# Performance work log

Measured on AMD Instinct MI355X. Metric: run time of the kernel, lower is better.

## Reference

```python
import jax, jax.numpy as jnp
import numpy as np

B, T, I = 16, 2048, 256   # batch, seq_len, input_size
H = 256                   # dcg hidden == trn hidden per layer
DF = 0.9                  # discount_factor


def _lstm_scan(x, Wih, bih, Whh, bhh, coeff):
    """LSTM scan over time with discount-coeff gating.
    x: [B,T,in], Wih: [4H,in], Whh: [4H,H], coeff: [B,T,1] (already zeroed at t=0).
    h_t = LSTMCell(x_t, h_{t-1}, c_{t-1}).h + coeff_t * h_{t-1}  (PyTorch gate order i,f,g,o).
    """
    xp = jnp.einsum('bti,gi->btg', x, Wih) + bih  # precompute input projections [B,T,4H]
    Hh = Whh.shape[1]
    h0 = jnp.zeros((x.shape[0], Hh), x.dtype)

    def step(carry, inp):
        h, c = carry
        xg, cf = inp
        g = xg + h @ Whh.T + bhh
        ii, ff, gg, oo = jnp.split(g, 4, axis=-1)
        cn = jax.nn.sigmoid(ff) * c + jax.nn.sigmoid(ii) * jnp.tanh(gg)
        hn = jax.nn.sigmoid(oo) * jnp.tanh(cn) + cf * h
        return (hn, cn), hn

    _, hs = jax.lax.scan(step, (h0, h0), (xp.swapaxes(0, 1), coeff.swapaxes(0, 1)))
    return hs.swapaxes(0, 1)  # [B,T,H]


def _forward(inputs, dWih_f, dWhh_f, dbih_f, dbhh_f, dWih_b, dWhh_b, dbih_b, dbhh_b,
             l0Wih_f, l0Whh_f, l0bih_f, l0bhh_f, l0Wih_b, l0Whh_b, l0bih_b, l0bhh_b,
             l1Wih_f, l1Whh_f, l1bih_f, l1bhh_f, l1Wih_b, l1Whh_b, l1bih_b, l1bhh_b,
             cw_f, cb_f, cw_b, cb_b):
    z = jnp.zeros(inputs.shape[:2] + (1,), inputs.dtype)
    # discount-coefficient generator: plain bidirectional LSTM (no gating)
    dof = _lstm_scan(inputs, dWih_f, dbih_f, dWhh_f, dbhh_f, z)
    dob = _lstm_scan(inputs[:, ::-1], dWih_b, dbih_b, dWhh_b, dbhh_b, z)[:, ::-1]
    fwc = DF * jax.nn.sigmoid(dof @ cw_f.T + cb_f)        # [B,T,1]
    bwc = DF * jax.nn.sigmoid(dob @ cw_b.T + cb_b)[:, ::-1]  # flipped, consumed in reversed time
    # coeff blending only applies for step index i > 0 in each direction's loop
    cf = fwc.at[:, 0].set(0.0)
    cb = bwc.at[:, 0].set(0.0)

    layers = [((l0Wih_f, l0bih_f, l0Whh_f, l0bhh_f), (l0Wih_b, l0bih_b, l0Whh_b, l0bhh_b)),
              ((l1Wih_f, l1bih_f, l1Whh_f, l1bhh_f), (l1Wih_b, l1bih_b, l1Whh_b, l1bhh_b))]
    x = inputs
    for pf, pb in layers:
        of = _lstm_scan(x, *pf, cf)
        ob = _lstm_scan(x[:, ::-1], *pb, cb)[:, ::-1]
        x = jnp.concatenate([of, ob], axis=-1)  # [B,T,2H]
    return x


def setup_inputs():
    key = jax.random.key(0)
    ki = iter(jax.random.split(key, 64))
    d = {"inputs": jax.random.normal(next(ki), (B, T, I), dtype=jnp.float32)}
    for pre, ind in [("d", I), ("l0", I), ("l1", 2 * H)]:
        for dr in ("f", "b"):
            d[f"{pre}Wih_{dr}"] = 0.05 * jax.random.normal(next(ki), (4 * H, ind), dtype=jnp.float32)
            d[f"{pre}Whh_{dr}"] = 0.05 * jax.random.normal(next(ki), (4 * H, H), dtype=jnp.float32)
            d[f"{pre}bih_{dr}"] = jnp.zeros((4 * H,), jnp.float32)
            d[f"{pre}bhh_{dr}"] = jnp.zeros((4 * H,), jnp.float32)
    for dr in ("f", "b"):
        d[f"cw_{dr}"] = 0.05 * jax.random.normal(next(ki), (1, H), dtype=jnp.float32)
        d[f"cb_{dr}"] = jnp.zeros((1,), jnp.float32)
    return d


def reference(inputs, dWih_f, dWhh_f, dbih_f, dbhh_f, dWih_b, dWhh_b, dbih_b, dbhh_b,
              l0Wih_f, l0Whh_f, l0bih_f, l0bhh_f, l0Wih_b, l0Whh_b, l0bih_b, l0bhh_b,
              l1Wih_f, l1Whh_f, l1bih_f, l1bhh_f, l1Wih_b, l1Whh_b, l1bih_b, l1bhh_b,
              cw_f, cb_f, cw_b, cb_b):
    return _forward(inputs, dWih_f, dWhh_f, dbih_f, dbhh_f, dWih_b, dWhh_b, dbih_b, dbhh_b,
                    l0Wih_f, l0Whh_f, l0bih_f, l0bhh_f, l0Wih_b, l0Whh_b, l0bih_b, l0bhh_b,
                    l1Wih_f, l1Whh_f, l1bih_f, l1bhh_f, l1Wih_b, l1Whh_b, l1bih_b, l1bhh_b,
                    cw_f, cb_f, cw_b, cb_b)
```

## Files before the change

kernel.cpp:

```cpp
#include <hip/hip_runtime.h>

typedef unsigned short ushort;
typedef unsigned int uint32;
typedef unsigned long long ull;
typedef __attribute__((ext_vector_type(8))) short bf16x8;
typedef __attribute__((ext_vector_type(4))) float f32x4;

#define BATCH 16
#define TT 2048
#define HID 256

__device__ __forceinline__ ushort f2bf(float f) {
  union { float f; uint32 u; } v; v.f = f;
  uint32 r = v.u + 0x7FFFu + ((v.u >> 16) & 1u);
  return (ushort)(r >> 16);
}
__device__ __forceinline__ float bf2f(ushort u) {
  union { uint32 u; float f; } v; v.u = ((uint32)u) << 16; return v.f;
}
__device__ __forceinline__ float sigm(float x) { return 1.0f / (1.0f + __expf(-x)); }
__device__ __forceinline__ float tanh_fast(float x) { return 1.0f - 2.0f / (__expf(2.0f * x) + 1.0f); }

__global__ void prep_kernel(
    const float* __restrict__ x,
    const float* __restrict__ l1Wih_f, const float* __restrict__ l1Wih_b,
    const float* __restrict__ dbih_f, const float* __restrict__ dbhh_f,
    const float* __restrict__ dbih_b, const float* __restrict__ dbhh_b,
    const float* __restrict__ l0bih_f, const float* __restrict__ l0bhh_f,
    const float* __restrict__ l0bih_b, const float* __restrict__ l0bhh_b,
    const float* __restrict__ l1bih_f, const float* __restrict__ l1bhh_f,
    const float* __restrict__ l1bih_b, const float* __restrict__ l1bhh_b,
    ushort* __restrict__ xbf, ushort* __restrict__ wC,
    float* __restrict__ biasA, float* __restrict__ biasB, float* __restrict__ biasC)
{
  int g = blockIdx.x * blockDim.x + threadIdx.x;
  int str = gridDim.x * blockDim.x;
  for (int i = g; i < (BATCH * TT * 256) / 4; i += str) {
    float4 v = ((const float4*)x)[i];
    ushort4 o; o.x = f2bf(v.x); o.y = f2bf(v.y); o.z = f2bf(v.z); o.w = f2bf(v.w);
    ((ushort4*)xbf)[i] = o;
  }
  for (int i = g; i < 2048 * 512; i += str)
    wC[i] = f2bf(i < 1024 * 512 ? l1Wih_f[i] : l1Wih_b[i - 1024 * 512]);
  for (int i = g; i < 2048; i += str) {
    biasA[i] = i < 1024 ? dbih_f[i] + dbhh_f[i] : dbih_b[i - 1024] + dbhh_b[i - 1024];
    biasB[i] = i < 1024 ? l0bih_f[i] + l0bhh_f[i] : l0bih_b[i - 1024] + l0bhh_b[i - 1024];
    biasC[i] = i < 1024 ? l1bih_f[i] + l1bhh_f[i] : l1bih_b[i - 1024] + l1bhh_b[i - 1024];
  }
}

__global__ __launch_bounds__(256) void gemm_xp(
    const ushort* __restrict__ A, const ushort* __restrict__ B, int K,
    const float* __restrict__ bias, ushort* __restrict__ xp)
{
  __shared__ __align__(16) ushort lA[128 * 64];
  __shared__ __align__(16) ushort lB[128 * 64];
  const int tid = threadIdx.x;
  const int lane = tid & 63, wv = tid >> 6;
  const int lo = lane & 15, hi = lane >> 4;
  const int wr = wv >> 1, wc = wv & 1;
  const int bm = blockIdx.y * 128, bn = blockIdx.x * 128;

  f32x4 acc[4][4] = {};

  const int nk = K >> 6;
  for (int kt = 0; kt < nk; ++kt) {
    uint4 ra[4], rb[4];
#pragma unroll
    for (int i = 0; i < 4; ++i) {
      int slot = i * 256 + tid;
      int r = slot >> 3, c8 = slot & 7;
      ra[i] = *(const uint4*)(A + (size_t)(bm + r) * K + kt * 64 + c8 * 8);
      rb[i] = *(const uint4*)(B + (size_t)(bn + r) * K + kt * 64 + c8 * 8);
    }
    __syncthreads();
#pragma unroll
    for (int i = 0; i < 4; ++i) {
      int slot = i * 256 + tid;
      int r = slot >> 3, c8 = slot & 7;
      int boff = r * 128 + ((c8 ^ (r & 7)) << 4);
      *(uint4*)((char*)lA + boff) = ra[i];
      *(uint4*)((char*)lB + boff) = rb[i];
    }
    __syncthreads();
#pragma unroll
    for (int kk = 0; kk < 2; ++kk) {
      bf16x8 fa[4], fb[4];
#pragma unroll
      for (int mt = 0; mt < 4; ++mt) {
        int r = wr * 64 + mt * 16 + lo;
        int c8 = kk * 4 + hi;
        fa[mt] = *(const bf16x8*)((const char*)lA + r * 128 + ((c8 ^ (r & 7)) << 4));
      }
#pragma unroll
      for (int nt = 0; nt < 4; ++nt) {
        int r = wc * 64 + nt * 16 + lo;
        int c8 = kk * 4 + hi;
        fb[nt] = *(const bf16x8*)((const char*)lB + r * 128 + ((c8 ^ (r & 7)) << 4));
      }
#pragma unroll
      for (int mt = 0; mt < 4; ++mt)
#pragma unroll
        for (int nt = 0; nt < 4; ++nt)
          acc[mt][nt] = __builtin_amdgcn_mfma_f32_16x16x32_bf16(fa[mt], fb[nt], acc[mt][nt], 0, 0, 0);
    }
  }
#pragma unroll
  for (int nt = 0; nt < 4; ++nt) {
    int n = bn + wc * 64 + nt * 16 + lo;
    float bv = bias[n];
    int dirn = n >> 10;
    int c = n & 1023;
    int gate = c >> 8;
    int u = c & 255;
    size_t base = (size_t)dirn * ((size_t)BATCH * TT * 1024) + (size_t)(u >> 1) * 8 + gate * 2;
#pragma unroll
    for (int mt = 0; mt < 4; ++mt) {
#pragma unroll
      for (int r = 0; r < 4; ++r) {
        float val = acc[mt][nt][r] + bv;
        uint32 h16 = f2bf(val);
        uint32 p16 = (uint32)__shfl_xor((int)h16, 1);
        if (!(lo & 1)) {
          int m = bm + wr * 64 + mt * 16 + hi * 4 + r;
          *(uint32*)(xp + base + (size_t)m * 1024) = h16 | (p16 << 16);
        }
      }
    }
  }
}

template <int MODE>
__device__ __forceinline__ void scan_fly(
    const ushort* __restrict__ xbf,
    const float* __restrict__ WihF, const float* __restrict__ WihB,
    const float* __restrict__ WhhF, const float* __restrict__ WhhB,
    const float* __restrict__ biasAll,
    const float* ldsCW, float cbias,
    ull* __restrict__ coefT,
    ull* __restrict__ hst_base,
    ushort* __restrict__ outBf,
    const int dir, const int w, const int tid)
{
  const int lane = tid & 63, wv = tid >> 6;
  const int lo = lane & 15, hi = lane >> 4;

  const float* Wih = dir ? WihB : WihF;
  const float* Whh = dir ? WhhB : WhhF;
  ull* hst = hst_base + dir * (2 * 2048);
  ull* coefD = coefT + (size_t)dir * TT * 16;

  const int unit = w * 64 + wv * 16 + lo;
  const int b0 = hi * 4;

  bf16x8 wih[4][8], whh[4][8];
#pragma unroll
  for (int gt = 0; gt < 4; ++gt) {
    const float* r1 = Wih + (size_t)(gt * HID + unit) * HID;
    const float* r2 = Whh + (size_t)(gt * HID + unit) * HID;
#pragma unroll
    for (int kt = 0; kt < 8; ++kt) {
      bf16x8 f1, f2;
#pragma unroll
      for (int j = 0; j < 8; ++j) {
        f1[j] = (short)f2bf(r1[kt * 32 + hi * 8 + j]);
        f2[j] = (short)f2bf(r2[kt * 32 + hi * 8 + j]);
      }
      wih[gt][kt] = f1; whh[gt][kt] = f2;
    }
  }
  float biasv[4];
#pragma unroll
  for (int gt = 0; gt < 4; ++gt) biasv[gt] = biasAll[dir * 1024 + gt * 256 + unit];

  float hprev[4] = {0, 0, 0, 0}, cprev[4] = {0, 0, 0, 0};
  float co[4] = {0, 0, 0, 0};

  uint4 xn[8];
  {
    const int t0 = dir ? (TT - 1) : 0;
    const ushort* p = xbf + ((size_t)lo * TT + t0) * 256 + hi * 8;
#pragma unroll
    for (int kt = 0; kt < 8; ++kt) xn[kt] = *(const uint4*)(p + kt * 32);
  }

  bf16x8 af[8];

  for (int s = 0; s < TT; ++s) {
    bf16x8 xa[8];
#pragma unroll
    for (int kt = 0; kt < 8; ++kt) {
      union { uint4 u; bf16x8 v; } t; t.u = xn[kt]; xa[kt] = t.v;
    }
    f32x4 acc[4];
#pragma unroll
    for (int gt = 0; gt < 4; ++gt) {
      acc[gt] = (f32x4){biasv[gt], biasv[gt], biasv[gt], biasv[gt]};
      acc[gt] = __builtin_amdgcn_mfma_f32_16x16x32_bf16(xa[0], wih[gt][0], acc[gt], 0, 0, 0);
      acc[gt] = __builtin_amdgcn_mfma_f32_16x16x32_bf16(xa[1], wih[gt][1], acc[gt], 0, 0, 0);
      acc[gt] = __builtin_amdgcn_mfma_f32_16x16x32_bf16(xa[2], wih[gt][2], acc[gt], 0, 0, 0);
      acc[gt] = __builtin_amdgcn_mfma_f32_16x16x32_bf16(xa[3], wih[gt][3], acc[gt], 0, 0, 0);
      acc[gt] = __builtin_amdgcn_mfma_f32_16x16x32_bf16(xa[4], wih[gt][4], acc[gt], 0, 0, 0);
      acc[gt] = __builtin_amdgcn_mfma_f32_16x16x32_bf16(xa[5], wih[gt][5], acc[gt], 0, 0, 0);
      acc[gt] = __builtin_amdgcn_mfma_f32_16x16x32_bf16(xa[6], wih[gt][6], acc[gt], 0, 0, 0);
      acc[gt] = __builtin_amdgcn_mfma_f32_16x16x32_bf16(xa[7], wih[gt][7], acc[gt], 0, 0, 0);
    }

    if (s + 1 < TT) {
      const int tn = dir ? (TT - 2 - s) : (s + 1);
      const ushort* p = xbf + ((size_t)lo * TT + tn) * 256 + hi * 8;
#pragma unroll
      for (int kt = 0; kt < 8; ++kt) xn[kt] = *(const uint4*)(p + kt * 32);
    }

    if (s > 0) {
      const ull* bp = hst + (s & 1) * 2048 + hi * 64 + lo;
      const ull* cp = coefD + (size_t)s * 16 + b0;
      const uint32 su = (uint32)s;
      while (true) {
        uint32 bad = 0;
#pragma unroll
        for (int kt = 0; kt < 8; ++kt) {
          ull w0 = __hip_atomic_load(bp + kt * 256 +  0, __ATOMIC_RELAXED, __HIP_MEMORY_SCOPE_AGENT);
          ull w1 = __hip_atomic_load(bp + kt * 256 + 16, __ATOMIC_RELAXED, __HIP_MEMORY_SCOPE_AGENT);
          ull w2 = __hip_atomic_load(bp + kt * 256 + 32, __ATOMIC_RELAXED, __HIP_MEMORY_SCOPE_AGENT);
          ull w3 = __hip_atomic_load(bp + kt * 256 + 48, __ATOMIC_RELAXED, __HIP_MEMORY_SCOPE_AGENT);
          union { bf16x8 v; uint32 d[4]; } t;
          t.d[0] = (uint32)w0; t.d[1] = (uint32)w1; t.d[2] = (uint32)w2; t.d[3] = (uint32)w3;
          af[kt] = t.v;
          bad |= ((uint32)(w0 >> 32)) ^ su; bad |= ((uint32)(w1 >> 32)) ^ su;
          bad |= ((uint32)(w2 >> 32)) ^ su; bad |= ((uint32)(w3 >> 32)) ^ su;
        }
        if (MODE == 1) {
          ull c0 = __hip_atomic_load(cp + 0, __ATOMIC_RELAXED, __HIP_MEMORY_SCOPE_AGENT);
          ull c1 = __hip_atomic_load(cp + 1, __ATOMIC_RELAXED, __HIP_MEMORY_SCOPE_AGENT);
          ull c2 = __hip_atomic_load(cp + 2, __ATOMIC_RELAXED, __HIP_MEMORY_SCOPE_AGENT);
          ull c3 = __hip_atomic_load(cp + 3, __ATOMIC_RELAXED, __HIP_MEMORY_SCOPE_AGENT);
          bad |= ((uint32)(c0 >> 32)) ^ (su + 1); bad |= ((uint32)(c1 >> 32)) ^ (su + 1);
          bad |= ((uint32)(c2 >> 32)) ^ (su + 1); bad |= ((uint32)(c3 >> 32)) ^ (su + 1);
          co[0] = __uint_as_float((uint32)c0); co[1] = __uint_as_float((uint32)c1);
          co[2] = __uint_as_float((uint32)c2); co[3] = __uint_as_float((uint32)c3);
        }
        if (__all(bad == 0)) break;
      }
#pragma unroll
      for (int gt = 0; gt < 4; ++gt) {
        acc[gt] = __builtin_amdgcn_mfma_f32_16x16x32_bf16(af[0], whh[gt][0], acc[gt], 0, 0, 0);
        acc[gt] = __builtin_amdgcn_mfma_f32_16x16x32_bf16(af[1], whh[gt][1], acc[gt], 0, 0, 0);
        acc[gt] = __builtin_amdgcn_mfma_f32_16x16x32_bf16(af[2], whh[gt][2], acc[gt], 0, 0, 0);
        acc[gt] = __builtin_amdgcn_mfma_f32_16x16x32_bf16(af[3], whh[gt][3], acc[gt], 0, 0, 0);
        acc[gt] = __builtin_amdgcn_mfma_f32_16x16x32_bf16(af[4], whh[gt][4], acc[gt], 0, 0, 0);
        acc[gt] = __builtin_amdgcn_mfma_f32_16x16x32_bf16(af[5], whh[gt][5], acc[gt], 0, 0, 0);
        acc[gt] = __builtin_amdgcn_mfma_f32_16x16x32_bf16(af[6], whh[gt][6], acc[gt], 0, 0, 0);
        acc[gt] = __builtin_amdgcn_mfma_f32_16x16x32_bf16(af[7], whh[gt][7], acc[gt], 0, 0, 0);
      }
    }

#pragma unroll
    for (int r = 0; r < 4; ++r) {
      float gi = acc[0][r];
      float gf = acc[1][r];
      float gg = acc[2][r];
      float go = acc[3][r];
      float cn = sigm(gf) * cprev[r] + sigm(gi) * tanh_fast(gg);
      float hn = sigm(go) * tanh_fast(cn) + co[r] * hprev[r];
      cprev[r] = cn; hprev[r] = hn;
    }

    {
      ull* so = hst + ((s + 1) & 1) * 2048 + (size_t)(w * 32 + wv * 8 + (lo >> 1)) * 16 + b0;
      const ull tg = ((ull)(uint32)(s + 1)) << 32;
#pragma unroll
      for (int r = 0; r < 4; ++r) {
        uint32 h16 = f2bf(hprev[r]);
        uint32 p16 = (uint32)__shfl_xor((int)h16, 1);
        if (!(lo & 1))
          __hip_atomic_store(so + r, (ull)(h16 | (p16 << 16)) | tg,
                             __ATOMIC_RELAXED, __HIP_MEMORY_SCOPE_AGENT);
      }
      asm volatile("" ::: "memory");
    }

    if (MODE == 0 && s > 0 && w == 0 && wv == 0) {
      float part = 0.f;
#pragma unroll
      for (int kt = 0; kt < 8; ++kt) {
        const float* cwp = &ldsCW[kt * 32 + hi * 8];
        f32x4 c0 = *(const f32x4*)cwp;
        f32x4 c1 = *(const f32x4*)(cwp + 4);
#pragma unroll
        for (int j = 0; j < 4; ++j) {
          part += c0[j] * bf2f((ushort)af[kt][j]);
          part += c1[j] * bf2f((ushort)af[kt][4 + j]);
        }
      }
      part += __shfl_xor(part, 16);
      part += __shfl_xor(part, 32);
      if (hi == 0) {
        uint32 pb = __float_as_uint(0.9f * sigm(part + cbias));
        __hip_atomic_store(coefD + (size_t)(s - 1) * 16 + lo, (((ull)(uint32)s) << 32) | pb,
                           __ATOMIC_RELAXED, __HIP_MEMORY_SCOPE_AGENT);
      }
      asm volatile("" ::: "memory");
    }

    if (MODE == 1) {
      const int t_nat = dir ? (TT - 1 - s) : s;
#pragma unroll
      for (int r = 0; r < 4; ++r)
        outBf[((size_t)(b0 + r) * TT + t_nat) * 512 + dir * 256 + unit] = f2bf(hprev[r]);
    }
  }

  if (MODE == 0 && w == 0 && wv == 0) {
    const ull* bp = hst + (TT & 1) * 2048 + hi * 64 + lo;
    const uint32 su = (uint32)TT;
    while (true) {
      uint32 bad = 0;
#pragma unroll
      for (int kt = 0; kt < 8; ++kt) {
        ull w0 = __hip_atomic_load(bp + kt * 256 +  0, __ATOMIC_RELAXED, __HIP_MEMORY_SCOPE_AGENT);
        ull w1 = __hip_atomic_load(bp + kt * 256 + 16, __ATOMIC_RELAXED, __HIP_MEMORY_SCOPE_AGENT);
        ull w2 = __hip_atomic_load(bp + kt * 256 + 32, __ATOMIC_RELAXED, __HIP_MEMORY_SCOPE_AGENT);
        ull w3 = __hip_atomic_load(bp + kt * 256 + 48, __ATOMIC_RELAXED, __HIP_MEMORY_SCOPE_AGENT);
        union { bf16x8 v; uint32 d[4]; } t;
        t.d[0] = (uint32)w0; t.d[1] = (uint32)w1; t.d[2] = (uint32)w2; t.d[3] = (uint32)w3;
        af[kt] = t.v;
        bad |= ((uint32)(w0 >> 32)) ^ su; bad |= ((uint32)(w1 >> 32)) ^ su;
        bad |= ((uint32)(w2 >> 32)) ^ su; bad |= ((uint32)(w3 >> 32)) ^ su;
      }
      if (__all(bad == 0)) break;
    }
    float part = 0.f;
#pragma unroll
    for (int kt = 0; kt < 8; ++kt) {
      const float* cwp = &ldsCW[kt * 32 + hi * 8];
      f32x4 c0 = *(const f32x4*)cwp;
      f32x4 c1 = *(const f32x4*)(cwp + 4);
#pragma unroll
      for (int j = 0; j < 4; ++j) {
        part += c0[j] * bf2f((ushort)af[kt][j]);
        part += c1[j] * bf2f((ushort)af[kt][4 + j]);
      }
    }
    part += __shfl_xor(part, 16);
    part += __shfl_xor(part, 32);
    if (hi == 0) {
      uint32 pb = __float_as_uint(0.9f * sigm(part + cbias));
      __hip_atomic_store(coefD + (size_t)(TT - 1) * 16 + lo, (((ull)(uint32)TT) << 32) | pb,
                         __ATOMIC_RELAXED, __HIP_MEMORY_SCOPE_AGENT);
    }
    asm volatile("" ::: "memory");
  }
}

__global__ __launch_bounds__(256, 1) void fused_AB(
    const ushort* __restrict__ xbf,
    const float* __restrict__ dWihF, const float* __restrict__ dWihB,
    const float* __restrict__ dWhhF, const float* __restrict__ dWhhB,
    const float* __restrict__ lWihF, const float* __restrict__ lWihB,
    const float* __restrict__ lWhhF, const float* __restrict__ lWhhB,
    const float* __restrict__ biasA, const float* __restrict__ biasB,
    const float* __restrict__ cwF, const float* __restrict__ cwB,
    const float* __restrict__ cbF, const float* __restrict__ cbB,
    ull* __restrict__ coefT, ull* __restrict__ hstA, ull* __restrict__ hstB,
    ushort* __restrict__ xcat)
{
  __shared__ float ldsCW[256];
  const int tid = threadIdx.x;
  const int role = blockIdx.x >> 3;
  const int dir = (blockIdx.x >> 2) & 1, w = blockIdx.x & 3;
  float cbias = 0.f;
  if (role == 0) { ldsCW[tid] = (dir ? cwB : cwF)[tid]; cbias = dir ? cbB[0] : cbF[0]; }
  __syncthreads();
  if (role == 0)
    scan_fly<0>(xbf, dWihF, dWihB, dWhhF, dWhhB, biasA, ldsCW, cbias,
                coefT, hstA, (ushort*)nullptr, dir, w, tid);
  else
    scan_fly<1>(xbf, lWihF, lWihB, lWhhF, lWhhB, biasB, ldsCW, 0.f,
                coefT, hstB, xcat, dir, w, tid);
}

__global__ __launch_bounds__(256, 1) void scan_l1(
    const ushort* __restrict__ xp,
    const float* __restrict__ WhhF, const float* __restrict__ WhhB,
    ull* __restrict__ coefT, ull* __restrict__ hst_base,
    float* __restrict__ outF32)
{
  const int tid = threadIdx.x;
  const int lane = tid & 63, wv = tid >> 6;
  const int lo = lane & 15, hi = lane >> 4;
  const int dir = blockIdx.x >> 2, w = blockIdx.x & 3;

  const ushort* xpD = xp + (size_t)dir * ((size_t)BATCH * TT * 1024);
  const float* Whh = dir ? WhhB : WhhF;
  ull* hst = hst_base + dir * (2 * 2048);
  ull* coefD = coefT + (size_t)dir * TT * 16;

  const int unit = w * 64 + wv * 16 + lo;
  const int b0 = hi * 4;
  const int sh = (unit & 1) * 16;

  bf16x8 wfrag[4][8];
#pragma unroll
  for (int gt = 0; gt < 4; ++gt) {
    const float* wrow = Whh + (size_t)(gt * HID + unit) * HID;
#pragma unroll
    for (int kt = 0; kt < 8; ++kt) {
      const float* p = wrow + kt * 32 + hi * 8;
      bf16x8 f;
#pragma unroll
      for (int j = 0; j < 8; ++j) f[j] = (short)f2bf(p[j]);
      wfrag[gt][kt] = f;
    }
  }

  float hprev[4] = {0, 0, 0, 0}, cprev[4] = {0, 0, 0, 0};
  float co[4] = {0, 0, 0, 0};
  uint4 xq0, xq1, xq2, xq3;
  {
    const int t0 = dir ? (TT - 1) : 0;
    const size_t pofs = (size_t)(unit >> 1) * 8;
    xq0 = *(const uint4*)(xpD + ((size_t)(b0 + 0) * TT + t0) * 1024 + pofs);
    xq1 = *(const uint4*)(xpD + ((size_t)(b0 + 1) * TT + t0) * 1024 + pofs);
    xq2 = *(const uint4*)(xpD + ((size_t)(b0 + 2) * TT + t0) * 1024 + pofs);
    xq3 = *(const uint4*)(xpD + ((size_t)(b0 + 3) * TT + t0) * 1024 + pofs);
  }

  bf16x8 af[8];
  for (int s = 0; s < TT; ++s) {
    float xgi[4], xgf[4], xgg[4], xgo[4];
#define XEXT(Q, R) \
    xgi[R] = bf2f((ushort)(Q.x >> sh)); xgf[R] = bf2f((ushort)(Q.y >> sh)); \
    xgg[R] = bf2f((ushort)(Q.z >> sh)); xgo[R] = bf2f((ushort)(Q.w >> sh));
    XEXT(xq0, 0) XEXT(xq1, 1) XEXT(xq2, 2) XEXT(xq3, 3)
#undef XEXT

    f32x4 acc[4] = {};
    if (s > 0) {
      const ull* bp = hst + (s & 1) * 2048 + hi * 64 + lo;
      const uint32 su = (uint32)s;
      while (true) {
        uint32 bad = 0;
#pragma unroll
        for (int kt = 0; kt < 8; ++kt) {
          ull w0 = __hip_atomic_load(bp + kt * 256 +  0, __ATOMIC_RELAXED, __HIP_MEMORY_SCOPE_AGENT);
          ull w1 = __hip_atomic_load(bp + kt * 256 + 16, __ATOMIC_RELAXED, __HIP_MEMORY_SCOPE_AGENT);
          ull w2 = __hip_atomic_load(bp + kt * 256 + 32, __ATOMIC_RELAXED, __HIP_MEMORY_SCOPE_AGENT);
          ull w3 = __hip_atomic_load(bp + kt * 256 + 48, __ATOMIC_RELAXED, __HIP_MEMORY_SCOPE_AGENT);
          union { bf16x8 v; uint32 d[4]; } t;
          t.d[0] = (uint32)w0; t.d[1] = (uint32)w1; t.d[2] = (uint32)w2; t.d[3] = (uint32)w3;
          af[kt] = t.v;
          bad |= ((uint32)(w0 >> 32)) ^ su; bad |= ((uint32)(w1 >> 32)) ^ su;
          bad |= ((uint32)(w2 >> 32)) ^ su; bad |= ((uint32)(w3 >> 32)) ^ su;
        }
        if (__all(bad == 0)) break;
      }
#pragma unroll
      for (int gt = 0; gt < 4; ++gt) {
        acc[gt] = __builtin_amdgcn_mfma_f32_16x16x32_bf16(af[0], wfrag[gt][0], acc[gt], 0, 0, 0);
        acc[gt] = __builtin_amdgcn_mfma_f32_16x16x32_bf16(af[1], wfrag[gt][1], acc[gt], 0, 0, 0);
        acc[gt] = __builtin_amdgcn_mfma_f32_16x16x32_bf16(af[2], wfrag[gt][2], acc[gt], 0, 0, 0);
        acc[gt] = __builtin_amdgcn_mfma_f32_16x16x32_bf16(af[3], wfrag[gt][3], acc[gt], 0, 0, 0);
        acc[gt] = __builtin_amdgcn_mfma_f32_16x16x32_bf16(af[4], wfrag[gt][4], acc[gt], 0, 0, 0);
        acc[gt] = __builtin_amdgcn_mfma_f32_16x16x32_bf16(af[5], wfrag[gt][5], acc[gt], 0, 0, 0);
        acc[gt] = __builtin_amdgcn_mfma_f32_16x16x32_bf16(af[6], wfrag[gt][6], acc[gt], 0, 0, 0);
        acc[gt] = __builtin_amdgcn_mfma_f32_16x16x32_bf16(af[7], wfrag[gt][7], acc[gt], 0, 0, 0);
      }
    }

#pragma unroll
    for (int r = 0; r < 4; ++r) {
      float gi = acc[0][r] + xgi[r];
      float gf = acc[1][r] + xgf[r];
      float gg = acc[2][r] + xgg[r];
      float go = acc[3][r] + xgo[r];
      float cn = sigm(gf) * cprev[r] + sigm(gi) * tanh_fast(gg);
      float hn = sigm(go) * tanh_fast(cn) + co[r] * hprev[r];
      cprev[r] = cn; hprev[r] = hn;
    }

    {
      ull* so = hst + ((s + 1) & 1) * 2048 + (size_t)(w * 32 + wv * 8 + (lo >> 1)) * 16 + b0;
      const ull tg = ((ull)(uint32)(s + 1)) << 32;
#pragma unroll
      for (int r = 0; r < 4; ++r) {
        uint32 h16 = f2bf(hprev[r]);
        uint32 p16 = (uint32)__shfl_xor((int)h16, 1);
        if (!(lo & 1))
          __hip_atomic_store(so + r, (ull)(h16 | (p16 << 16)) | tg,
                             __ATOMIC_RELAXED, __HIP_MEMORY_SCOPE_AGENT);
      }
      asm volatile("" ::: "memory");
    }

    const int t_nat = dir ? (TT - 1 - s) : s;
#pragma unroll
    for (int r = 0; r < 4; ++r)
      outF32[((size_t)(b0 + r) * TT + t_nat) * 512 + dir * 256 + unit] = hprev[r];

    if (s + 1 < TT) {
      const int tn = dir ? (TT - 2 - s) : (s + 1);
      const size_t pofs = (size_t)(unit >> 1) * 8;
      xq0 = *(const uint4*)(xpD + ((size_t)(b0 + 0) * TT + tn) * 1024 + pofs);
      xq1 = *(const uint4*)(xpD + ((size_t)(b0 + 1) * TT + tn) * 1024 + pofs);
      xq2 = *(const uint4*)(xpD + ((size_t)(b0 + 2) * TT + tn) * 1024 + pofs);
      xq3 = *(const uint4*)(xpD + ((size_t)(b0 + 3) * TT + tn) * 1024 + pofs);
      co[0] = __uint_as_float((uint32)coefD[(size_t)(s + 1) * 16 + b0 + 0]);
      co[1] = __uint_as_float((uint32)coefD[(size_t)(s + 1) * 16 + b0 + 1]);
      co[2] = __uint_as_float((uint32)coefD[(size_t)(s + 1) * 16 + b0 + 2]);
      co[3] = __uint_as_float((uint32)coefD[(size_t)(s + 1) * 16 + b0 + 3]);
    }
  }
}

extern "C" void kernel_launch(void* const* d_in, const int* in_sizes, int n_in,
                              void* d_out, int out_size, void* d_ws, size_t ws_size,
                              hipStream_t stream)
{
  const float* x       = (const float*)d_in[0];
  const float* dWih_f  = (const float*)d_in[1];
  const float* dWhh_f  = (const float*)d_in[2];
  const float* dbih_f  = (const float*)d_in[3];
  const float* dbhh_f  = (const float*)d_in[4];
  const float* dWih_b  = (const float*)d_in[5];
  const float* dWhh_b  = (const float*)d_in[6];
  const float* dbih_b  = (const float*)d_in[7];
  const float* dbhh_b  = (const float*)d_in[8];
  const float* l0Wih_f = (const float*)d_in[9];
  const float* l0Whh_f = (const float*)d_in[10];
  const float* l0bih_f = (const float*)d_in[11];
  const float* l0bhh_f = (const float*)d_in[12];
  const float* l0Wih_b = (const float*)d_in[13];
  const float* l0Whh_b = (const float*)d_in[14];
  const float* l0bih_b = (const float*)d_in[15];
  const float* l0bhh_b = (const float*)d_in[16];
  const float* l1Wih_f = (const float*)d_in[17];
  const float* l1Whh_f = (const float*)d_in[18];
  const float* l1bih_f = (const float*)d_in[19];
  const float* l1bhh_f = (const float*)d_in[20];
  const float* l1Wih_b = (const float*)d_in[21];
  const float* l1Whh_b = (const float*)d_in[22];
  const float* l1bih_b = (const float*)d_in[23];
  const float* l1bhh_b = (const float*)d_in[24];
  const float* cw_f    = (const float*)d_in[25];
  const float* cbi_f   = (const float*)d_in[26];
  const float* cw_b    = (const float*)d_in[27];
  const float* cbi_b   = (const float*)d_in[28];

  char* ws = (char*)d_ws;
  constexpr size_t OFF_XP   = 0;
  constexpr size_t SZ_XP    = 2ull * BATCH * TT * 1024 * 2;
  constexpr size_t OFF_XCAT = OFF_XP + SZ_XP;
  constexpr size_t SZ_XCAT  = (size_t)BATCH * TT * 512 * 2;
  constexpr size_t OFF_XBF  = OFF_XCAT + SZ_XCAT;
  constexpr size_t SZ_XBF   = (size_t)BATCH * TT * 256 * 2;
  constexpr size_t OFF_WC   = OFF_XBF + SZ_XBF;
  constexpr size_t SZ_WC    = 2048ull * 512 * 2;
  constexpr size_t OFF_BA   = OFF_WC + SZ_WC;
  constexpr size_t OFF_BB   = OFF_BA + 8192;
  constexpr size_t OFF_BC   = OFF_BB + 8192;
  constexpr size_t OFF_CO   = OFF_BC + 8192;
  constexpr size_t SZ_CO    = 2ull * TT * 16 * 8;
  constexpr size_t OFF_HST  = OFF_CO + SZ_CO;
  constexpr size_t SZ_HST   = 3ull * 2 * 2 * 2048 * 8;
  constexpr size_t NEED     = OFF_HST + SZ_HST;
  if (ws_size < NEED) return;

  ushort* xp    = (ushort*)(ws + OFF_XP);
  ushort* xcat  = (ushort*)(ws + OFF_XCAT);
  ushort* xbf   = (ushort*)(ws + OFF_XBF);
  ushort* wC    = (ushort*)(ws + OFF_WC);
  float*  biasA = (float*)(ws + OFF_BA);
  float*  biasB = (float*)(ws + OFF_BB);
  float*  biasC = (float*)(ws + OFF_BC);
  ull*    coefT = (ull*)(ws + OFF_CO);
  ull*    hst   = (ull*)(ws + OFF_HST);

  prep_kernel<<<512, 256, 0, stream>>>(
      x, l1Wih_f, l1Wih_b,
      dbih_f, dbhh_f, dbih_b, dbhh_b, l0bih_f, l0bhh_f, l0bih_b, l0bhh_b,
      l1bih_f, l1bhh_f, l1bih_b, l1bhh_b,
      xbf, wC, biasA, biasB, biasC);
  hipMemsetAsync(ws + OFF_CO, 0, SZ_CO + SZ_HST, stream);

  const size_t HSTR = 2 * 2 * 2048;

  fused_AB<<<16, 256, 0, stream>>>(xbf,
                                   dWih_f, dWih_b, dWhh_f, dWhh_b,
                                   l0Wih_f, l0Wih_b, l0Whh_f, l0Whh_b,
                                   biasA, biasB, cw_f, cw_b, cbi_f, cbi_b,
                                   coefT, hst + 0 * HSTR, hst + 1 * HSTR, xcat);
  gemm_xp<<<dim3(16, 256), 256, 0, stream>>>(xcat, wC, 512, biasC, xp);
  scan_l1<<<8, 256, 0, stream>>>(xp, l1Whh_f, l1Whh_b, coefT, hst + 2 * HSTR, (float*)d_out);
}
```

Measured before the change: 18.48 ms.

## Split layer-1 scan across two blocks per direction with LDS-local hidden state

The layer-1 recurrent scan now uses 2 blocks per direction instead of 4. Each wave handles 32 hidden units, and each block keeps its own half of h in swizzled LDS, so only the other block's half is polled through global atomics. The aim is to cut cross-block handshake traffic and latency on the serial per-step critical path. In exchange, each wave does twice the MFMA work and register pressure rises, and a __syncthreads is added every step. s_sleep backoff is also added to all spin-wait loops to reduce polling contention.

Measured after the change: 19.91 ms. +7.7%, slower.

```diff
diff --git a/kernel.cpp b/kernel.cpp
--- a/kernel.cpp
+++ b/kernel.cpp
@@ -242,6 +242,7 @@
           co[2] = __uint_as_float((uint32)c2); co[3] = __uint_as_float((uint32)c3);
         }
         if (__all(bad == 0)) break;
+        __builtin_amdgcn_s_sleep(1);
       }
 #pragma unroll
       for (int gt = 0; gt < 4; ++gt) {
@@ -330,6 +331,7 @@
         bad |= ((uint32)(w2 >> 32)) ^ su; bad |= ((uint32)(w3 >> 32)) ^ su;
       }
       if (__all(bad == 0)) break;
+      __builtin_amdgcn_s_sleep(1);
     }
     float part = 0.f;
 #pragma unroll
@@ -390,122 +392,168 @@
   const int tid = threadIdx.x;
   const int lane = tid & 63, wv = tid >> 6;
   const int lo = lane & 15, hi = lane >> 4;
-  const int dir = blockIdx.x >> 2, w = blockIdx.x & 3;
+  const int dir = blockIdx.x >> 1, w = blockIdx.x & 1;
+
+  __shared__ __align__(16) ushort ldsH[2][16 * 128];
 
   const ushort* xpD = xp + (size_t)dir * ((size_t)BATCH * TT * 1024);
   const float* Whh = dir ? WhhB : WhhF;
   ull* hst = hst_base + dir * (2 * 2048);
   ull* coefD = coefT + (size_t)dir * TT * 16;
 
-  const int unit = w * 64 + wv * 16 + lo;
+  const int ub = w * 128 + wv * 32;
   const int b0 = hi * 4;
-  const int sh = (unit & 1) * 16;
-
-  bf16x8 wfrag[4][8];
+  const int sh = (lo & 1) * 16;
+
+  bf16x8 wfrag[4][2][8];
 #pragma unroll
   for (int gt = 0; gt < 4; ++gt) {
-    const float* wrow = Whh + (size_t)(gt * HID + unit) * HID;
-#pragma unroll
-    for (int kt = 0; kt < 8; ++kt) {
-      const float* p = wrow + kt * 32 + hi * 8;
-      bf16x8 f;
-#pragma unroll
-      for (int j = 0; j < 8; ++j) f[j] = (short)f2bf(p[j]);
-      wfrag[gt][kt] = f;
-    }
-  }
-
-  float hprev[4] = {0, 0, 0, 0}, cprev[4] = {0, 0, 0, 0};
+#pragma unroll
+    for (int ug = 0; ug < 2; ++ug) {
+      const float* wrow = Whh + (size_t)(gt * HID + ub + ug * 16 + lo) * HID;
+#pragma unroll
+      for (int kt = 0; kt < 8; ++kt) {
+        bf16x8 f;
+#pragma unroll
+        for (int j = 0; j < 8; ++j) f[j] = (short)f2bf(wrow[kt * 32 + hi * 8 + j]);
+        wfrag[gt][ug][kt] = f;
+      }
+    }
+  }
+
+  float hprev[2][4] = {}, cprev[2][4] = {};
   float co[4] = {0, 0, 0, 0};
-  uint4 xq0, xq1, xq2, xq3;
+  uint4 xq[2][4];
   {
     const int t0 = dir ? (TT - 1) : 0;
-    const size_t pofs = (size_t)(unit >> 1) * 8;
-    xq0 = *(const uint4*)(xpD + ((size_t)(b0 + 0) * TT + t0) * 1024 + pofs);
-    xq1 = *(const uint4*)(xpD + ((size_t)(b0 + 1) * TT + t0) * 1024 + pofs);
-    xq2 = *(const uint4*)(xpD + ((size_t)(b0 + 2) * TT + t0) * 1024 + pofs);
-    xq3 = *(const uint4*)(xpD + ((size_t)(b0 + 3) * TT + t0) * 1024 + pofs);
-  }
-
-  bf16x8 af[8];
+#pragma unroll
+    for (int ug = 0; ug < 2; ++ug) {
+      const size_t pofs = (size_t)((ub + ug * 16 + lo) >> 1) * 8;
+#pragma unroll
+      for (int r = 0; r < 4; ++r)
+        xq[ug][r] = *(const uint4*)(xpD + ((size_t)(b0 + r) * TT + t0) * 1024 + pofs);
+    }
+  }
+
   for (int s = 0; s < TT; ++s) {
-    float xgi[4], xgf[4], xgg[4], xgo[4];
-#define XEXT(Q, R) \
-    xgi[R] = bf2f((ushort)(Q.x >> sh)); xgf[R] = bf2f((ushort)(Q.y >> sh)); \
-    xgg[R] = bf2f((ushort)(Q.z >> sh)); xgo[R] = bf2f((ushort)(Q.w >> sh));
-    XEXT(xq0, 0) XEXT(xq1, 1) XEXT(xq2, 2) XEXT(xq3, 3)
-#undef XEXT
-
-    f32x4 acc[4] = {};
+    f32x4 acc[4][2] = {};
     if (s > 0) {
+      bf16x8 af0, af1, af2, af3, af4, af5, af6, af7;
+      const char* lb = (const char*)ldsH + (s & 1) * 4096 + lo * 256;
+      const int lx = (lo & 7) << 4;
       const ull* bp = hst + (s & 1) * 2048 + hi * 64 + lo;
       const uint32 su = (uint32)s;
-      while (true) {
-        uint32 bad = 0;
-#pragma unroll
-        for (int kt = 0; kt < 8; ++kt) {
-          ull w0 = __hip_atomic_load(bp + kt * 256 +  0, __ATOMIC_RELAXED, __HIP_MEMORY_SCOPE_AGENT);
-          ull w1 = __hip_atomic_load(bp + kt * 256 + 16, __ATOMIC_RELAXED, __HIP_MEMORY_SCOPE_AGENT);
-          ull w2 = __hip_atomic_load(bp + kt * 256 + 32, __ATOMIC_RELAXED, __HIP_MEMORY_SCOPE_AGENT);
-          ull w3 = __hip_atomic_load(bp + kt * 256 + 48, __ATOMIC_RELAXED, __HIP_MEMORY_SCOPE_AGENT);
-          union { bf16x8 v; uint32 d[4]; } t;
-          t.d[0] = (uint32)w0; t.d[1] = (uint32)w1; t.d[2] = (uint32)w2; t.d[3] = (uint32)w3;
-          af[kt] = t.v;
-          bad |= ((uint32)(w0 >> 32)) ^ su; bad |= ((uint32)(w1 >> 32)) ^ su;
-          bad |= ((uint32)(w2 >> 32)) ^ su; bad |= ((uint32)(w3 >> 32)) ^ su;
-        }
-        if (__all(bad == 0)) break;
-      }
+
+#define LDK(KT, A) { \
+        ull w0 = __hip_atomic_load(bp + KT * 256 +  0, __ATOMIC_RELAXED, __HIP_MEMORY_SCOPE_AGENT); \
+        ull w1 = __hip_atomic_load(bp + KT * 256 + 16, __ATOMIC_RELAXED, __HIP_MEMORY_SCOPE_AGENT); \
+        ull w2 = __hip_atomic_load(bp + KT * 256 + 32, __ATOMIC_RELAXED, __HIP_MEMORY_SCOPE_AGENT); \
+        ull w3 = __hip_atomic_load(bp + KT * 256 + 48, __ATOMIC_RELAXED, __HIP_MEMORY_SCOPE_AGENT); \
+        union { bf16x8 v; uint32 d[4]; } t; \
+        t.d[0] = (uint32)w0; t.d[1] = (uint32)w1; t.d[2] = (uint32)w2; t.d[3] = (uint32)w3; \
+        A = t.v; \
+        bad |= ((uint32)(w0 >> 32)) ^ su; bad |= ((uint32)(w1 >> 32)) ^ su; \
+        bad |= ((uint32)(w2 >> 32)) ^ su; bad |= ((uint32)(w3 >> 32)) ^ su; }
+
+      if (w == 0) {
+        af0 = *(const bf16x8*)(lb + ((0 * 64 + hi * 16) ^ lx));
+        af1 = *(const bf16x8*)(lb + ((1 * 64 + hi * 16) ^ lx));
+        af2 = *(const bf16x8*)(lb + ((2 * 64 + hi * 16) ^ lx));
+        af3 = *(const bf16x8*)(lb + ((3 * 64 + hi * 16) ^ lx));
+        while (true) {
+          uint32 bad = 0;
+          LDK(4, af4) LDK(5, af5) LDK(6, af6) LDK(7, af7)
+          if (__all(bad == 0)) break;
+          __builtin_amdgcn_s_sleep(1);
+        }
+      } else {
+        af4 = *(const bf16x8*)(lb + ((0 * 64 + hi * 16) ^ lx));
+        af5 = *(const bf16x8*)(lb + ((1 * 64 + hi * 16) ^ lx));
+        af6 = *(const bf16x8*)(lb + ((2 * 64 + hi * 16) ^ lx));
+        af7 = *(const bf16x8*)(lb + ((3 * 64 + hi * 16) ^ lx));
+        while (true) {
+          uint32 bad = 0;
+          LDK(0, af0) LDK(1, af1) LDK(2, af2) LDK(3, af3)
+          if (__all(bad == 0)) break;
+          __builtin_amdgcn_s_sleep(1);
+        }
+      }
+#undef LDK
+
 #pragma unroll
       for (int gt = 0; gt < 4; ++gt) {
-        acc[gt] = __builtin_amdgcn_mfma_f32_16x16x32_bf16(af[0], wfrag[gt][0], acc[gt], 0, 0, 0);
-        acc[gt] = __builtin_amdgcn_mfma_f32_16x16x32_bf16(af[1], wfrag[gt][1], acc[gt], 0, 0, 0);
-        acc[gt] = __builtin_amdgcn_mfma_f32_16x16x32_bf16(af[2], wfrag[gt][2], acc[gt], 0, 0, 0);
-        acc[gt] = __builtin_amdgcn_mfma_f32_16x16x32_bf16(af[3], wfrag[gt][3], acc[gt], 0, 0, 0);
-        acc[gt] = __builtin_amdgcn_mfma_f32_16x16x32_bf16(af[4], wfrag[gt][4], acc[gt], 0, 0, 0);
-        acc[gt] = __builtin_amdgcn_mfma_f32_16x16x32_bf16(af[5], wfrag[gt][5], acc[gt], 0, 0, 0);
-        acc[gt] = __builtin_amdgcn_mfma_f32_16x16x32_bf16(af[6], wfrag[gt][6], acc[gt], 0, 0, 0);
-        acc[gt] = __builtin_amdgcn_mfma_f32_16x16x32_bf16(af[7], wfrag[gt][7], acc[gt], 0, 0, 0);
-      }
-    }
-
-#pragma unroll
-    for (int r = 0; r < 4; ++r) {
-      float gi = acc[0][r] + xgi[r];
-      float gf = acc[1][r] + xgf[r];
-      float gg = acc[2][r] + xgg[r];
-      float go = acc[3][r] + xgo[r];
-      float cn = sigm(gf) * cprev[r] + sigm(gi) * tanh_fast(gg);
-      float hn = sigm(go) * tanh_fast(cn) + co[r] * hprev[r];
-      cprev[r] = cn; hprev[r] = hn;
+#pragma unroll
+        for (int ug = 0; ug < 2; ++ug) {
+          acc[gt][ug] = __builtin_amdgcn_mfma_f32_16x16x32_bf16(af0, wfrag[gt][ug][0], acc[gt][ug], 0, 0, 0);
+          acc[gt][ug] = __builtin_amdgcn_mfma_f32_16x16x32_bf16(af1, wfrag[gt][ug][1], acc[gt][ug], 0, 0, 0);
+          acc[gt][ug] = __builtin_amdgcn_mfma_f32_16x16x32_bf16(af2, wfrag[gt][ug][2], acc[gt][ug], 0, 0, 0);
+          acc[gt][ug] = __builtin_amdgcn_mfma_f32_16x16x32_bf16(af3, wfrag[gt][ug][3], acc[gt][ug], 0, 0, 0);
+          acc[gt][ug] = __builtin_amdgcn_mfma_f32_16x16x32_bf16(af4, wfrag[gt][ug][4], acc[gt][ug], 0, 0, 0);
+          acc[gt][ug] = __builtin_amdgcn_mfma_f32_16x16x32_bf16(af5, wfrag[gt][ug][5], acc[gt][ug], 0, 0, 0);
+          acc[gt][ug] = __builtin_amdgcn_mfma_f32_16x16x32_bf16(af6, wfrag[gt][ug][6], acc[gt][ug], 0, 0, 0);
+          acc[gt][ug] = __builtin_amdgcn_mfma_f32_16x16x32_bf16(af7, wfrag[gt][ug][7], acc[gt][ug], 0, 0, 0);
+        }
+      }
+    }
+
+#pragma unroll
+    for (int ug = 0; ug < 2; ++ug) {
+#pragma unroll
+      for (int r = 0; r < 4; ++r) {
+        uint4 q = xq[ug][r];
+        float gi = acc[0][ug][r] + bf2f((ushort)(q.x >> sh));
+        float gf = acc[1][ug][r] + bf2f((ushort)(q.y >> sh));
+        float gg = acc[2][ug][r] + bf2f((ushort)(q.z >> sh));
+        float go = acc[3][ug][r] + bf2f((ushort)(q.w >> sh));
+        float cn = sigm(gf) * cprev[ug][r] + sigm(gi) * tanh_fast(gg);
+        float hn = sigm(go) * tanh_fast(cn) + co[r] * hprev[ug][r];
+        cprev[ug][r] = cn; hprev[ug][r] = hn;
+      }
     }
 
     {
-      ull* so = hst + ((s + 1) & 1) * 2048 + (size_t)(w * 32 + wv * 8 + (lo >> 1)) * 16 + b0;
+      const int nb = (s + 1) & 1;
       const ull tg = ((ull)(uint32)(s + 1)) << 32;
 #pragma unroll
-      for (int r = 0; r < 4; ++r) {
-        uint32 h16 = f2bf(hprev[r]);
-        uint32 p16 = (uint32)__shfl_xor((int)h16, 1);
-        if (!(lo & 1))
-          __hip_atomic_store(so + r, (ull)(h16 | (p16 << 16)) | tg,
-                             __ATOMIC_RELAXED, __HIP_MEMORY_SCOPE_AGENT);
+      for (int ug = 0; ug < 2; ++ug) {
+#pragma unroll
+        for (int r = 0; r < 4; ++r) {
+          uint32 h16 = f2bf(hprev[ug][r]);
+          uint32 p16 = (uint32)__shfl_xor((int)h16, 1);
+          if (!(lo & 1)) {
+            uint32 pk = h16 | (p16 << 16);
+            int p = (ub + ug * 16 + lo) >> 1;
+            __hip_atomic_store(hst + nb * 2048 + (size_t)p * 16 + (b0 + r),
+                               (ull)pk | tg, __ATOMIC_RELAXED, __HIP_MEMORY_SCOPE_AGENT);
+            int ulocal = wv * 32 + ug * 16 + lo;
+            int bo = nb * 4096 + (b0 + r) * 256 + ulocal * 2;
+            bo ^= (((b0 + r) & 7) << 4);
+            *(uint32*)((char*)ldsH + bo) = pk;
+          }
+        }
       }
       asm volatile("" ::: "memory");
     }
-
-    const int t_nat = dir ? (TT - 1 - s) : s;
-#pragma unroll
-    for (int r = 0; r < 4; ++r)
-      outF32[((size_t)(b0 + r) * TT + t_nat) * 512 + dir * 256 + unit] = hprev[r];
+    __syncthreads();
+
+    {
+      const int t_nat = dir ? (TT - 1 - s) : s;
+#pragma unroll
+      for (int ug = 0; ug < 2; ++ug)
+#pragma unroll
+        for (int r = 0; r < 4; ++r)
+          outF32[((size_t)(b0 + r) * TT + t_nat) * 512 + dir * 256 + ub + ug * 16 + lo] = hprev[ug][r];
+    }
 
     if (s + 1 < TT) {
       const int tn = dir ? (TT - 2 - s) : (s + 1);
-      const size_t pofs = (size_t)(unit >> 1) * 8;
-      xq0 = *(const uint4*)(xpD + ((size_t)(b0 + 0) * TT + tn) * 1024 + pofs);
-      xq1 = *(const uint4*)(xpD + ((size_t)(b0 + 1) * TT + tn) * 1024 + pofs);
-      xq2 = *(const uint4*)(xpD + ((size_t)(b0 + 2) * TT + tn) * 1024 + pofs);
-      xq3 = *(const uint4*)(xpD + ((size_t)(b0 + 3) * TT + tn) * 1024 + pofs);
+#pragma unroll
+      for (int ug = 0; ug < 2; ++ug) {
+        const size_t pofs = (size_t)((ub + ug * 16 + lo) >> 1) * 8;
+#pragma unroll
+        for (int r = 0; r < 4; ++r)
+          xq[ug][r] = *(const uint4*)(xpD + ((size_t)(b0 + r) * TT + tn) * 1024 + pofs);
+      }
       co[0] = __uint_as_float((uint32)coefD[(size_t)(s + 1) * 16 + b0 + 0]);
       co[1] = __uint_as_float((uint32)coefD[(size_t)(s + 1) * 16 + b0 + 1]);
       co[2] = __uint_as_float((uint32)coefD[(size_t)(s + 1) * 16 + b0 + 2]);
@@ -592,5 +640,5 @@
                                    biasA, biasB, cw_f, cw_b, cbi_f, cbi_b,
                                    coefT, hst + 0 * HSTR, hst + 1 * HSTR, xcat);
   gemm_xp<<<dim3(16, 256), 256, 0, stream>>>(xcat, wC, 512, biasC, xp);
-  scan_l1<<<8, 256, 0, stream>>>(xp, l1Whh_f, l1Whh_b, coefT, hst + 2 * HSTR, (float*)d_out);
-}
+  scan_l1<<<4, 256, 0, stream>>>(xp, l1Whh_f, l1Whh_b, coefT, hst + 2 * HSTR, (float*)d_out);
+}
```
